# Kernel optimization log

Hardware: AMD Instinct MI355X
Metric: run time of the kernel (lower is better)

The kernel has to match this reference:

```python
import jax, jax.numpy as jnp
import numpy as np

B, S, D = 8, 4096, 192
MEM_READ, MEM_WRITE, MEM_READY = 156, 157, 158


def setup_inputs() -> dict:
    key = jax.random.key(0)
    ks = jax.random.split(key, 9)
    inp = {"x": jax.random.normal(ks[0], (B, S, D), dtype=jnp.float32)}
    names = ["Wq_r", "Wk_r", "Wv_r", "Wo_r", "Wq_w", "Wk_w", "Wv_w", "Wo_w"]
    for i, n in enumerate(names):
        inp[n] = jax.random.normal(ks[i + 1], (D, D), dtype=jnp.float32) * 0.02
    return inp


def _attention(x, Wq, Wk, Wv, Wo):
    # single-head, non-causal PureAttention: q/k/v = x @ W.T, softmax(qk^T/sqrt(D)) v, then W_o
    q = jnp.einsum('bsd,ed->bse', x, Wq)
    k = jnp.einsum('bsd,ed->bse', x, Wk)
    v = jnp.einsum('bsd,ed->bse', x, Wv)
    scale = jnp.asarray(1.0 / np.sqrt(D), x.dtype)
    scores = jnp.einsum('bqe,bke->bqk', q, k) * scale  # [B,S,S]
    attn = jax.nn.softmax(scores, axis=-1)
    o = jnp.einsum('bqk,bke->bqe', attn, v)
    return jnp.einsum('bse,oe->bso', o, Wo)


def reference(x, Wq_r, Wk_r, Wv_r, Wo_r, Wq_w, Wk_w, Wv_w, Wo_w):
    read_flag = x[:, 0, MEM_READ]    # [B]
    write_flag = x[:, 0, MEM_WRITE]  # [B]
    read_res = _attention(x, Wq_r, Wk_r, Wv_r, Wo_r)
    write_res = _attention(x, Wq_w, Wk_w, Wv_w, Wo_w)
    rg = read_flag[:, None, None]
    wg = write_flag[:, None, None]
    out = x + rg * (read_res - x) + wg * (write_res - x)
    out = out.at[:, :, MEM_READ].set(0.0)
    out = out.at[:, :, MEM_WRITE].set(0.0)
    ready = (read_flag + write_flag)[:, None]  # broadcast over seq
    out = out.at[:, :, MEM_READY].set(jnp.broadcast_to(ready, out.shape[:2]))
    return out
```

## Files before the change

kernel.cpp:

```cpp
#include <hip/hip_runtime.h>
#include <stdint.h>

#define B_ 8
#define S_ 4096
#define D_ 192
#define M_ (B_*S_)
#define VTILE 7680

typedef short v8s __attribute__((ext_vector_type(8)));
typedef float v4f __attribute__((ext_vector_type(4)));
typedef unsigned short v4us __attribute__((ext_vector_type(4)));
typedef unsigned long long ull;

static __device__ __forceinline__ unsigned short f2bf(float f){
  union{float f; unsigned u;} v; v.f=f;
  unsigned u = v.u;
  unsigned r = (u + 0x7fffu + ((u>>16)&1u))>>16;
  return (unsigned short)r;
}
static __device__ __forceinline__ float fexp2(float x){
  return __builtin_amdgcn_exp2f(x);
}
static __device__ __forceinline__ unsigned cvtpk(float lo, float hi){
  unsigned r;
  asm("v_cvt_pk_bf16_f32 %0, %1, %2" : "=v"(r) : "v"(lo), "v"(hi));
  return r;
}
static __device__ __forceinline__ float asf(unsigned u){
  union{unsigned u; float f;} v; v.u=u; return v.f;
}

static __device__ __forceinline__ unsigned sw_fp8(float x){
  union{float f; unsigned u;} v; v.f = x;
  unsigned s = (v.u >> 24) & 0x80u;
  float a = fabsf(x);
  if (a < 0.001953125f) return s;
  if (a >= 240.f) return s | 0x7Eu;
  if (a < 0.015625f) {
    int m = (int)(a*512.f + 0.5f); if(m>7) m=7;
    return s | (unsigned)m;
  }
  int e = (int)((v.u >> 23) & 0xff) - 127;
  unsigned mant = (v.u >> 20) & 0x7u;
  unsigned rest = v.u & 0xFFFFFu;
  if (rest > 0x80000u || (rest == 0x80000u && (mant&1u))) mant++;
  unsigned ee = (unsigned)(e + 7);
  if (mant == 8u){ mant = 0u; ee++; }
  return s | (ee<<3) | mant;
}
template<bool HI>
static __device__ __forceinline__ unsigned pk8(float a, float b, unsigned old){
#if __has_builtin(__builtin_amdgcn_cvt_pk_fp8_f32)
  return __builtin_amdgcn_cvt_pk_fp8_f32(a, b, old, HI);
#else
  unsigned p = sw_fp8(a) | (sw_fp8(b)<<8);
  return HI ? ((old & 0x0000FFFFu) | (p<<16)) : ((old & 0xFFFF0000u) | p);
#endif
}

typedef const __attribute__((address_space(1))) unsigned int gu32;
typedef __attribute__((address_space(3))) unsigned int lu32;
#define GLL16(gp, lp) __builtin_amdgcn_global_load_lds((gu32*)(gp), (lu32*)(lp), 16, 0, 0)

__global__ void cvt_w_kernel(const float* w0,const float* w1,const float* w2,const float* w3,
                             const float* w4,const float* w5,const float* w6,const float* w7,
                             unsigned short* dst){
  int w = blockIdx.y;
  const float* src;
  switch(w){
    case 0: src=w0; break; case 1: src=w1; break; case 2: src=w2; break; case 3: src=w3; break;
    case 4: src=w4; break; case 5: src=w5; break; case 6: src=w6; break; default: src=w7; break;
  }
  int i = blockIdx.x*256 + threadIdx.x;
  float v = src[i];
  if(w==0 || w==4 || w==1 || w==5) v *= 0.32267249f;
  dst[(size_t)w*36864 + i] = f2bf(v);
}

__global__ __launch_bounds__(256) void proj_kernel(
    const float* __restrict__ x, const unsigned short* __restrict__ Wb,
    unsigned char* __restrict__ QK8, unsigned char* __restrict__ V8)
{
  __shared__ __align__(16) unsigned char Vstage8[2*VTILE];
  const size_t MDB = (size_t)M_*D_;
  int path = blockIdx.y;
  int tid = threadIdx.x;
  int wid = tid>>6, lane = tid&63;
  int lr = lane&15, lg = lane>>4, kb = lg*8;
  int m0 = blockIdx.x*64 + wid*16;
  int row = m0 + lr;

  v8s a[6];
  #pragma unroll
  for(int c=0;c<6;c++){
    const float* xp = &x[(size_t)row*D_ + c*32 + kb];
    float4 f0 = *(const float4*)xp;
    float4 f1 = *(const float4*)(xp+4);
    v8s t;
    t[0]=(short)f2bf(f0.x); t[1]=(short)f2bf(f0.y); t[2]=(short)f2bf(f0.z); t[3]=(short)f2bf(f0.w);
    t[4]=(short)f2bf(f1.x); t[5]=(short)f2bf(f1.y); t[6]=(short)f2bf(f1.z); t[7]=(short)f2bf(f1.w);
    a[c]=t;
  }
  int bidx = m0 / S_;
  int sb   = (blockIdx.x*64) % S_;
  int sloc = wid*16 + lg*4;

  unsigned char* dstQ8 = QK8 + (size_t)path*2*MDB;
  for(int which=0; which<2; which++){
    const unsigned short* W = Wb + (size_t)(path*4 + which)*36864;
    unsigned char* dst = which==0 ? dstQ8 : dstQ8 + MDB;
    #pragma unroll
    for(int nt=0; nt<12; nt++){
      v4f acc = {0.f,0.f,0.f,0.f};
      int n = nt*16 + lr;
      #pragma unroll
      for(int c=0;c<6;c++){
        v8s bfr = *(const v8s*)&W[(size_t)n*D_ + c*32 + kb];
        acc = __builtin_amdgcn_mfma_f32_16x16x32_bf16(a[c], bfr, acc, 0,0,0);
      }
      int col = nt*16 + lr;
      int r0 = m0 + lg*4;
      #pragma unroll
      for(int r=0;r<4;r++){
        unsigned p = pk8<false>(acc[r], 0.f, 0u);
        dst[(size_t)(r0+r)*D_ + col] = (unsigned char)(p & 0xFF);
      }
    }
  }
  {
    const unsigned short* W = Wb + (size_t)(path*4 + 2)*36864;
    int t2 = sloc >> 5, s32 = sloc & 31;
    #pragma unroll
    for(int nt=0; nt<12; nt++){
      v4f acc = {0.f,0.f,0.f,0.f};
      int n = nt*16 + lr;
      #pragma unroll
      for(int c=0;c<6;c++){
        v8s bfr = *(const v8s*)&W[(size_t)n*D_ + c*32 + kb];
        acc = __builtin_amdgcn_mfma_f32_16x16x32_bf16(a[c], bfr, acc, 0,0,0);
      }
      int col = nt*16 + lr;
      unsigned pk4 = pk8<false>(acc[0], acc[1], 0u);
      pk4 = pk8<true>(acc[2], acc[3], pk4);
      *(unsigned*)&Vstage8[t2*VTILE + col*40 + s32] = pk4;
    }
    __syncthreads();
    unsigned char* dstV = V8 + (size_t)path*((size_t)B_*128*VTILE)
                        + ((size_t)bidx*128 + (sb>>5))*VTILE;
    #pragma unroll
    for(int j=0;j<4;j++){
      int i = tid + j*256;
      if(i<960) *(v8s*)&dstV[i*16] = *(const v8s*)&Vstage8[i*16];
    }
  }
}

#define KSTR8 200

__global__ __launch_bounds__(512,4) void attn_kernel(
    const unsigned char* __restrict__ QK8,
    const unsigned char* __restrict__ V8,
    unsigned short* __restrict__ Ob)
{
  __shared__ __align__(16) unsigned char KL[2][32*KSTR8];
  __shared__ __align__(16) unsigned char VL8[3][VTILE];

  int flat = blockIdx.x + 32*blockIdx.y + 256*blockIdx.z;
  int w = (flat&7)*64 + (flat>>3);
  int qi = w & 31;
  int b  = (w>>5) & 7;
  int z  = w>>8;

  const size_t MDB = (size_t)M_*D_;
  const unsigned char* Q8 = QK8 + (size_t)z*2*MDB;
  const unsigned char* K8 = Q8 + MDB;
  const unsigned char* Vp = V8 + (size_t)z*((size_t)B_*128*VTILE);
  unsigned short* O = Ob + (size_t)z*MDB;

  int q0 = qi*128;
  int tid = threadIdx.x, wid=tid>>6, lane=tid&63;
  int lr = lane&15, lg = lane>>4;
  size_t bK = (size_t)b*S_*D_;
  int qrow0 = q0 + wid*16;

  bool isK = wid < 4;
  int kt256 = tid & 255;
  int ksR = kt256>>3, ksC = (kt256&7)*24;
  int kLds = ksR*KSTR8 + ksC;

  long qf8[6];
  {
    const unsigned char* qp = Q8 + bK + (size_t)(qrow0 + lr)*D_;
    #pragma unroll
    for(int c=0;c<6;c++) qf8[c] = *(const long*)(qp + c*32 + lg*8);
  }
  float lsum = 0.f;
  v4f oacc[12];
  #pragma unroll
  for(int e=0;e<12;e++) oacc[e] = (v4f){0.f,0.f,0.f,0.f};

  ull k0, k1, k2;
  auto kissue = [&](int t){
    if(isK){
      const unsigned char* kg = K8 + bK + (size_t)t*6144 + ksR*192 + ksC;
      k0 = *(const ull*)(kg);
      k1 = *(const ull*)(kg+8);
      k2 = *(const ull*)(kg+16);
    }
  };
  auto kwrite = [&](int buf){
    if(isK){
      unsigned char* d = &KL[buf][kLds];
      *(ull*)(d)    = k0;
      *(ull*)(d+8)  = k1;
      *(ull*)(d+16) = k2;
    }
  };
  auto vissue = [&](int t, int buf){
    if(!isK){
      const unsigned char* vg = Vp + ((size_t)b*128 + t)*VTILE;
      #pragma unroll
      for(int j=0;j<2;j++){
        int i = (tid&255) + j*256;
        if(i<480) GLL16(vg + i*16, &VL8[buf][i*16]);
      }
    }
  };
  auto do_qk = [&](int kcur, v4f sacc[2]){
    __builtin_amdgcn_s_setprio(1);
    #pragma unroll
    for(int ct=0; ct<2; ct++){
      v4f s = {0.f,0.f,0.f,0.f};
      const unsigned char* rb = &KL[kcur][(ct*16+lr)*KSTR8];
      #pragma unroll
      for(int c=0;c<6;c++){
        long kf8 = *(const long*)(rb + c*32 + lg*8);
        s = __builtin_amdgcn_mfma_f32_16x16x32_fp8_fp8(kf8, qf8[c], s, 0,0,0);
      }
      sacc[ct]=s;
    }
    __builtin_amdgcn_s_setprio(0);
  };
  auto do_softmax = [&](v4f sacc[2], long& pa8){
    float p00=fexp2(sacc[0][0]), p01=fexp2(sacc[0][1]);
    float p02=fexp2(sacc[0][2]), p03=fexp2(sacc[0][3]);
    float p10=fexp2(sacc[1][0]), p11=fexp2(sacc[1][1]);
    float p12=fexp2(sacc[1][2]), p13=fexp2(sacc[1][3]);
    lsum += ((p00+p01)+(p02+p03)) + ((p10+p11)+(p12+p13));
    unsigned X0=cvtpk(p00,p01), X1=cvtpk(p02,p03);
    unsigned Y0=cvtpk(p10,p11), Y1=cvtpk(p12,p13);
    asm("v_permlane32_swap_b32 %0, %1" : "+v"(Y0), "+v"(X0));
    asm("v_permlane32_swap_b32 %0, %1" : "+v"(Y1), "+v"(X1));
    asm("v_permlane16_swap_b32 %0, %1" : "+v"(Y0), "+v"(X0));
    asm("v_permlane16_swap_b32 %0, %1" : "+v"(Y1), "+v"(X1));
    float e0 = asf(X0<<16), e1 = asf(X0 & 0xffff0000u);
    float e2 = asf(X1<<16), e3 = asf(X1 & 0xffff0000u);
    float e4 = asf(Y0<<16), e5 = asf(Y0 & 0xffff0000u);
    float e6 = asf(Y1<<16), e7 = asf(Y1 & 0xffff0000u);
    unsigned lo = pk8<false>(e0,e1,0u); lo = pk8<true>(e2,e3,lo);
    unsigned hi = pk8<false>(e4,e5,0u); hi = pk8<true>(e6,e7,hi);
    pa8 = (long)(((ull)hi<<32) | (ull)lo);
  };
  auto do_pv = [&](int vcur, long pa8){
    __builtin_amdgcn_s_setprio(1);
    #pragma unroll
    for(int e=0;e<12;e++){
      long vb8 = *(const long*)&VL8[vcur][(e*16+lr)*40 + lg*8];
      oacc[e] = __builtin_amdgcn_mfma_f32_16x16x32_fp8_fp8(pa8, vb8, oacc[e], 0,0,0);
    }
    __builtin_amdgcn_s_setprio(0);
  };

  kissue(0);
  vissue(0, 0);
  kwrite(0);
  asm volatile("s_waitcnt vmcnt(0)" ::: "memory");
  __syncthreads();

  long pa_prev;
  {
    v4f sacc[2];
    do_qk(0, sacc);
    kissue(1);
    vissue(1, 1);
    __builtin_amdgcn_sched_barrier(0);
    do_softmax(sacc, pa_prev);
    kwrite(1);
    asm volatile("s_waitcnt vmcnt(0)" ::: "memory");
    __syncthreads();
  }

  for(int t=1; t<128; t++){
    v4f sacc[2];
    do_qk(t&1, sacc);
    if(t<127){ kissue(t+1); vissue(t+1, (t+1)%3); }
    __builtin_amdgcn_sched_barrier(0);
    do_pv((t-1)%3, pa_prev);
    do_softmax(sacc, pa_prev);
    if(t<127) kwrite((t+1)&1);
    asm volatile("s_waitcnt vmcnt(0)" ::: "memory");
    __syncthreads();
  }
  do_pv(127%3, pa_prev);

  float ps = lsum;
  ps += __shfl_xor(ps, 16);
  ps += __shfl_xor(ps, 32);
  float iv = 1.0f/ps;
  float invr[4];
  #pragma unroll
  for(int r=0;r<4;r++) invr[r] = __shfl(iv, lg*4+r, 16);
  size_t orow0 = ((size_t)b*S_ + qrow0 + lg*4)*D_;
  #pragma unroll
  for(int e=0;e<12;e++){
    #pragma unroll
    for(int r=0;r<4;r++){
      O[orow0 + (size_t)r*D_ + e*16 + lr] = f2bf(oacc[e][r]*invr[r]);
    }
  }
}

__global__ __launch_bounds__(256) void final_kernel(
  const float* __restrict__ x,
  const unsigned short* __restrict__ Or,
  const unsigned short* __restrict__ Ow,
  const unsigned short* __restrict__ WoR,
  const unsigned short* __restrict__ WoW,
  float* __restrict__ out)
{
  int halfn = blockIdx.y;
  int tid=threadIdx.x, wid=tid>>6, lane=tid&63;
  int lr=lane&15, lg=lane>>4, kb=lg*8;
  int m0 = blockIdx.x*64 + wid*16;
  int arow = m0 + lr;
  v8s ar[6], aw[6];
  #pragma unroll
  for(int c=0;c<6;c++){
    ar[c] = *(const v8s*)&Or[(size_t)arow*D_ + c*32 + kb];
    aw[c] = *(const v8s*)&Ow[(size_t)arow*D_ + c*32 + kb];
  }
  int bidx = m0 / S_;
  float rf = x[(size_t)bidx*S_*D_ + 156];
  float wf = x[(size_t)bidx*S_*D_ + 157];
  #pragma unroll
  for(int ntl=0; ntl<6; ntl++){
    int nt = halfn*6 + ntl;
    v4f accR={0.f,0.f,0.f,0.f}, accW={0.f,0.f,0.f,0.f};
    int n = nt*16 + lr;
    #pragma unroll
    for(int c=0;c<6;c++){
      v8s br = *(const v8s*)&WoR[(size_t)n*D_ + c*32 + kb];
      accR = __builtin_amdgcn_mfma_f32_16x16x32_bf16(ar[c], br, accR,0,0,0);
      v8s bw = *(const v8s*)&WoW[(size_t)n*D_ + c*32 + kb];
      accW = __builtin_amdgcn_mfma_f32_16x16x32_bf16(aw[c], bw, accW,0,0,0);
    }
    #pragma unroll
    for(int r=0;r<4;r++){
      int row = m0 + lg*4 + r;
      int col = nt*16 + lr;
      float xv = x[(size_t)row*D_ + col];
      float val = xv + rf*(accR[r]-xv) + wf*(accW[r]-xv);
      if(col==156||col==157) val = 0.f;
      else if(col==158) val = rf+wf;
      out[(size_t)row*D_ + col] = val;
    }
  }
}

extern "C" void kernel_launch(void* const* d_in, const int* in_sizes, int n_in,
                              void* d_out, int out_size, void* d_ws, size_t ws_size,
                              hipStream_t stream) {
  const float* x = (const float*)d_in[0];
  char* wsb = (char*)d_ws;
  const size_t WSZ = 36864;
  const size_t MDB = (size_t)M_*D_;
  const size_t V8SZ = (size_t)2*B_*128*VTILE;
  unsigned short* Wb  = (unsigned short*)wsb;
  unsigned char*  QK8 = (unsigned char*)(wsb + 8*WSZ*2);
  unsigned char*  V8  = QK8 + 4*MDB;
  unsigned short* Ob  = (unsigned short*)(V8 + V8SZ);

  cvt_w_kernel<<<dim3(144,8),256,0,stream>>>(
      (const float*)d_in[1],(const float*)d_in[2],(const float*)d_in[3],(const float*)d_in[4],
      (const float*)d_in[5],(const float*)d_in[6],(const float*)d_in[7],(const float*)d_in[8], Wb);

  proj_kernel<<<dim3(512,2),256,0,stream>>>(x, Wb, QK8, V8);
  attn_kernel<<<dim3(32,8,2),512,0,stream>>>(QK8, V8, Ob);
  final_kernel<<<dim3(512,2),256,0,stream>>>(x, Ob, Ob + MDB,
                                             Wb+3*WSZ, Wb+7*WSZ, (float*)d_out);
}
```

Baseline: 309.9 us.

## Pre-tile K in LDS-padded layout and stage K via direct global-to-LDS loads

The projection kernel now writes K in per-32-row tiles already padded to the LDS stride, so the attention kernel can stage K with direct global-to-LDS 16-byte loads instead of loading into registers and writing to LDS. All 512 threads share the K and V staging instead of splitting by wave. The softmax packing is also simplified: probabilities are packed to fp8 first and then lane-swapped, dropping the bf16 intermediate and half the permlane swaps. The padded K layout uses slightly more workspace and gives the projection kernel scattered byte stores.

```diff
diff --git a/kernel.cpp b/kernel.cpp
--- a/kernel.cpp
+++ b/kernel.cpp
@@ -6,10 +6,10 @@
 #define D_ 192
 #define M_ (B_*S_)
 #define VTILE 7680
+#define KTILE 6400
 
 typedef short v8s __attribute__((ext_vector_type(8)));
 typedef float v4f __attribute__((ext_vector_type(4)));
-typedef unsigned short v4us __attribute__((ext_vector_type(4)));
 typedef unsigned long long ull;
 
 static __device__ __forceinline__ unsigned short f2bf(float f){
@@ -20,14 +20,6 @@
 }
 static __device__ __forceinline__ float fexp2(float x){
   return __builtin_amdgcn_exp2f(x);
-}
-static __device__ __forceinline__ unsigned cvtpk(float lo, float hi){
-  unsigned r;
-  asm("v_cvt_pk_bf16_f32 %0, %1, %2" : "=v"(r) : "v"(lo), "v"(hi));
-  return r;
-}
-static __device__ __forceinline__ float asf(unsigned u){
-  union{unsigned u; float f;} v; v.u=u; return v.f;
 }
 
 static __device__ __forceinline__ unsigned sw_fp8(float x){
@@ -79,7 +71,8 @@
 
 __global__ __launch_bounds__(256) void proj_kernel(
     const float* __restrict__ x, const unsigned short* __restrict__ Wb,
-    unsigned char* __restrict__ QK8, unsigned char* __restrict__ V8)
+    unsigned char* __restrict__ Q8g, unsigned char* __restrict__ K8t,
+    unsigned char* __restrict__ V8)
 {
   __shared__ __align__(16) unsigned char Vstage8[2*VTILE];
   const size_t MDB = (size_t)M_*D_;
@@ -105,10 +98,9 @@
   int sb   = (blockIdx.x*64) % S_;
   int sloc = wid*16 + lg*4;
 
-  unsigned char* dstQ8 = QK8 + (size_t)path*2*MDB;
-  for(int which=0; which<2; which++){
-    const unsigned short* W = Wb + (size_t)(path*4 + which)*36864;
-    unsigned char* dst = which==0 ? dstQ8 : dstQ8 + MDB;
+  {
+    const unsigned short* W = Wb + (size_t)(path*4 + 0)*36864;
+    unsigned char* dst = Q8g + (size_t)path*MDB;
     #pragma unroll
     for(int nt=0; nt<12; nt++){
       v4f acc = {0.f,0.f,0.f,0.f};
@@ -124,6 +116,27 @@
       for(int r=0;r<4;r++){
         unsigned p = pk8<false>(acc[r], 0.f, 0u);
         dst[(size_t)(r0+r)*D_ + col] = (unsigned char)(p & 0xFF);
+      }
+    }
+  }
+  {
+    const unsigned short* W = Wb + (size_t)(path*4 + 1)*36864;
+    unsigned char* dstK = K8t + ((size_t)path*B_ + bidx)*128*KTILE;
+    #pragma unroll
+    for(int nt=0; nt<12; nt++){
+      v4f acc = {0.f,0.f,0.f,0.f};
+      int n = nt*16 + lr;
+      #pragma unroll
+      for(int c=0;c<6;c++){
+        v8s bfr = *(const v8s*)&W[(size_t)n*D_ + c*32 + kb];
+        acc = __builtin_amdgcn_mfma_f32_16x16x32_bf16(a[c], bfr, acc, 0,0,0);
+      }
+      int col = nt*16 + lr;
+      #pragma unroll
+      for(int r=0;r<4;r++){
+        int rowS = sb + sloc + r;
+        unsigned p = pk8<false>(acc[r], 0.f, 0u);
+        dstK[(size_t)(rowS>>5)*KTILE + (rowS&31)*200 + col] = (unsigned char)(p & 0xFF);
       }
     }
   }
@@ -158,11 +171,12 @@
 #define KSTR8 200
 
 __global__ __launch_bounds__(512,4) void attn_kernel(
-    const unsigned char* __restrict__ QK8,
+    const unsigned char* __restrict__ Q8g,
+    const unsigned char* __restrict__ K8t,
     const unsigned char* __restrict__ V8,
     unsigned short* __restrict__ Ob)
 {
-  __shared__ __align__(16) unsigned char KL[2][32*KSTR8];
+  __shared__ __align__(16) unsigned char KL[2][KTILE];
   __shared__ __align__(16) unsigned char VL8[3][VTILE];
 
   int flat = blockIdx.x + 32*blockIdx.y + 256*blockIdx.z;
@@ -172,9 +186,9 @@
   int z  = w>>8;
 
   const size_t MDB = (size_t)M_*D_;
-  const unsigned char* Q8 = QK8 + (size_t)z*2*MDB;
-  const unsigned char* K8 = Q8 + MDB;
-  const unsigned char* Vp = V8 + (size_t)z*((size_t)B_*128*VTILE);
+  const unsigned char* Q8 = Q8g + (size_t)z*MDB;
+  const unsigned char* Kp = K8t + ((size_t)z*B_ + b)*128*KTILE;
+  const unsigned char* Vp = V8 + (size_t)z*((size_t)B_*128*VTILE) + (size_t)b*128*VTILE;
   unsigned short* O = Ob + (size_t)z*MDB;
 
   int q0 = qi*128;
@@ -183,10 +197,8 @@
   size_t bK = (size_t)b*S_*D_;
   int qrow0 = q0 + wid*16;
 
-  bool isK = wid < 4;
-  int kt256 = tid & 255;
-  int ksR = kt256>>3, ksC = (kt256&7)*24;
-  int kLds = ksR*KSTR8 + ksC;
+  bool doK = tid < 400;
+  bool doV = tid < 480;
 
   long qf8[6];
   {
@@ -199,32 +211,9 @@
   #pragma unroll
   for(int e=0;e<12;e++) oacc[e] = (v4f){0.f,0.f,0.f,0.f};
 
-  ull k0, k1, k2;
-  auto kissue = [&](int t){
-    if(isK){
-      const unsigned char* kg = K8 + bK + (size_t)t*6144 + ksR*192 + ksC;
-      k0 = *(const ull*)(kg);
-      k1 = *(const ull*)(kg+8);
-      k2 = *(const ull*)(kg+16);
-    }
-  };
-  auto kwrite = [&](int buf){
-    if(isK){
-      unsigned char* d = &KL[buf][kLds];
-      *(ull*)(d)    = k0;
-      *(ull*)(d+8)  = k1;
-      *(ull*)(d+16) = k2;
-    }
-  };
-  auto vissue = [&](int t, int buf){
-    if(!isK){
-      const unsigned char* vg = Vp + ((size_t)b*128 + t)*VTILE;
-      #pragma unroll
-      for(int j=0;j<2;j++){
-        int i = (tid&255) + j*256;
-        if(i<480) GLL16(vg + i*16, &VL8[buf][i*16]);
-      }
-    }
+  auto stage = [&](int t, int kbuf, int vbuf){
+    if(doK) GLL16(Kp + (size_t)t*KTILE + tid*16, &KL[kbuf][tid*16]);
+    if(doV) GLL16(Vp + (size_t)t*VTILE + tid*16, &VL8[vbuf][tid*16]);
   };
   auto do_qk = [&](int kcur, v4f sacc[2]){
     __builtin_amdgcn_s_setprio(1);
@@ -247,19 +236,11 @@
     float p10=fexp2(sacc[1][0]), p11=fexp2(sacc[1][1]);
     float p12=fexp2(sacc[1][2]), p13=fexp2(sacc[1][3]);
     lsum += ((p00+p01)+(p02+p03)) + ((p10+p11)+(p12+p13));
-    unsigned X0=cvtpk(p00,p01), X1=cvtpk(p02,p03);
-    unsigned Y0=cvtpk(p10,p11), Y1=cvtpk(p12,p13);
-    asm("v_permlane32_swap_b32 %0, %1" : "+v"(Y0), "+v"(X0));
-    asm("v_permlane32_swap_b32 %0, %1" : "+v"(Y1), "+v"(X1));
-    asm("v_permlane16_swap_b32 %0, %1" : "+v"(Y0), "+v"(X0));
-    asm("v_permlane16_swap_b32 %0, %1" : "+v"(Y1), "+v"(X1));
-    float e0 = asf(X0<<16), e1 = asf(X0 & 0xffff0000u);
-    float e2 = asf(X1<<16), e3 = asf(X1 & 0xffff0000u);
-    float e4 = asf(Y0<<16), e5 = asf(Y0 & 0xffff0000u);
-    float e6 = asf(Y1<<16), e7 = asf(Y1 & 0xffff0000u);
-    unsigned lo = pk8<false>(e0,e1,0u); lo = pk8<true>(e2,e3,lo);
-    unsigned hi = pk8<false>(e4,e5,0u); hi = pk8<true>(e6,e7,hi);
-    pa8 = (long)(((ull)hi<<32) | (ull)lo);
+    unsigned A = pk8<false>(p00,p01,0u); A = pk8<true>(p02,p03,A);
+    unsigned Bx= pk8<false>(p10,p11,0u); Bx= pk8<true>(p12,p13,Bx);
+    asm("v_permlane32_swap_b32 %0, %1" : "+v"(Bx), "+v"(A));
+    asm("v_permlane16_swap_b32 %0, %1" : "+v"(Bx), "+v"(A));
+    pa8 = (long)(((ull)Bx<<32) | (ull)A);
   };
   auto do_pv = [&](int vcur, long pa8){
     __builtin_amdgcn_s_setprio(1);
@@ -271,9 +252,7 @@
     __builtin_amdgcn_s_setprio(0);
   };
 
-  kissue(0);
-  vissue(0, 0);
-  kwrite(0);
+  stage(0, 0, 0);
   asm volatile("s_waitcnt vmcnt(0)" ::: "memory");
   __syncthreads();
 
@@ -281,11 +260,9 @@
   {
     v4f sacc[2];
     do_qk(0, sacc);
-    kissue(1);
-    vissue(1, 1);
+    stage(1, 1, 1);
     __builtin_amdgcn_sched_barrier(0);
     do_softmax(sacc, pa_prev);
-    kwrite(1);
     asm volatile("s_waitcnt vmcnt(0)" ::: "memory");
     __syncthreads();
   }
@@ -293,11 +270,10 @@
   for(int t=1; t<128; t++){
     v4f sacc[2];
     do_qk(t&1, sacc);
-    if(t<127){ kissue(t+1); vissue(t+1, (t+1)%3); }
+    if(t<127) stage(t+1, (t+1)&1, (t+1)%3);
     __builtin_amdgcn_sched_barrier(0);
     do_pv((t-1)%3, pa_prev);
     do_softmax(sacc, pa_prev);
-    if(t<127) kwrite((t+1)&1);
     asm volatile("s_waitcnt vmcnt(0)" ::: "memory");
     __syncthreads();
   }
@@ -374,18 +350,20 @@
   char* wsb = (char*)d_ws;
   const size_t WSZ = 36864;
   const size_t MDB = (size_t)M_*D_;
+  const size_t K8SZ = (size_t)2*B_*128*KTILE;
   const size_t V8SZ = (size_t)2*B_*128*VTILE;
   unsigned short* Wb  = (unsigned short*)wsb;
-  unsigned char*  QK8 = (unsigned char*)(wsb + 8*WSZ*2);
-  unsigned char*  V8  = QK8 + 4*MDB;
+  unsigned char*  Q8  = (unsigned char*)(wsb + 8*WSZ*2);
+  unsigned char*  K8t = Q8 + 2*MDB;
+  unsigned char*  V8  = K8t + K8SZ;
   unsigned short* Ob  = (unsigned short*)(V8 + V8SZ);
 
   cvt_w_kernel<<<dim3(144,8),256,0,stream>>>(
       (const float*)d_in[1],(const float*)d_in[2],(const float*)d_in[3],(const float*)d_in[4],
       (const float*)d_in[5],(const float*)d_in[6],(const float*)d_in[7],(const float*)d_in[8], Wb);
 
-  proj_kernel<<<dim3(512,2),256,0,stream>>>(x, Wb, QK8, V8);
-  attn_kernel<<<dim3(32,8,2),512,0,stream>>>(QK8, V8, Ob);
+  proj_kernel<<<dim3(512,2),256,0,stream>>>(x, Wb, Q8, K8t, V8);
+  attn_kernel<<<dim3(32,8,2),512,0,stream>>>(Q8, K8t, V8, Ob);
   final_kernel<<<dim3(512,2),256,0,stream>>>(x, Ob, Ob + MDB,
                                              Wb+3*WSZ, Wb+7*WSZ, (float*)d_out);
 }
```

New measurement: 298.8 us. -3.6%, faster.
